# Kernel tuning notes

Measured on AMD Instinct MI355X. Metric: run time of the kernel, lower is better.

The kernel has to match this reference:

```python
import jax, jax.numpy as jnp
import numpy as np

N = 50000      # nodes
E = 800000     # edges (avg degree 16)
D_IN = 128
D_H = 128
D_OUT = 64
SLOPE = 0.2    # leaky-relu negative slope (from the 0.2 constants in the graph)


def setup_inputs() -> dict:
    key = jax.random.key(0)
    ks = jax.random.split(key, 18)
    def w(k, shape, fan_in):
        return jax.random.normal(k, shape, jnp.float32) / np.sqrt(fan_in)
    inp = {
        "x": jax.random.normal(ks[0], (N, D_IN), jnp.float32),
        "W0": w(ks[1], (D_IN, D_H), D_IN),
        "b0": jnp.zeros((D_H,), jnp.float32),
        "Wq1": w(ks[2], (D_H, D_H), D_H),
        "bq1": jnp.zeros((D_H,), jnp.float32),
        "Wp1": w(ks[3], (D_H, D_H), D_H),
        "bp1": jnp.zeros((D_H,), jnp.float32),
        "a1": 0.1 * w(ks[4], (D_H,), D_H),
        "bg2": jnp.zeros((D_H,), jnp.float32),
        "Wq2": w(ks[5], (D_H, D_OUT), D_H),
        "bq2": jnp.zeros((D_OUT,), jnp.float32),
        "Wp2": w(ks[6], (D_H, D_OUT), D_H),
        "bp2": jnp.zeros((D_OUT,), jnp.float32),
        "a2": 0.1 * w(ks[7], (D_OUT,), D_OUT),
        "b_out": jnp.zeros((D_OUT,), jnp.float32),
        "src": jax.random.randint(ks[8], (E,), 0, N),
        "dst": jax.random.randint(ks[9], (E,), 0, N),
        "num_nodes": N,
    }
    return inp


def _gat_block(m, src, dst, Wq, bq, Wp, bp, a, n):
    # m: [N, d_in]; q/p: [N, d]
    q = m @ Wq + bq
    p = m @ Wp + bp
    # edge scores: s_e = sum_d leaky_relu(q[dst_e] + p[src_e]) * a_d   [E]
    e = jax.nn.leaky_relu(q[dst] + p[src], SLOPE)          # [E, d]
    s = jnp.einsum("ed,d->e", e, a)                        # [E]
    es = jnp.exp(s)                                        # unstabilized exp, as in source graph
    denom = jax.ops.segment_sum(es, dst, num_segments=n)   # [N]
    alpha = es / denom[dst]                                # [E] edge softmax over incoming edges
    # aggregate messages alpha_e * p[src_e] into dst nodes
    agg = jax.ops.segment_sum(alpha[:, None] * p[src], dst, num_segments=n)  # [N, d]
    return agg


def reference(x, W0, b0, Wq1, bq1, Wp1, bp1, a1, bg2, Wq2, bq2, Wp2, bp2, a2, b_out, src, dst, num_nodes):
    m1 = jax.nn.gelu(x @ W0 + b0, approximate=False)       # erf GELU per graph constants
    h1 = _gat_block(m1, src, dst, Wq1, bq1, Wp1, bp1, a1, num_nodes)
    m2 = jax.nn.gelu(h1 + bg2, approximate=False)
    h2 = _gat_block(m2, src, dst, Wq2, bq2, Wp2, bp2, a2, num_nodes)
    return h2 + b_out
```

## Files before the change

kernel.cpp:

```cpp
#include <hip/hip_runtime.h>
#include <hip/hip_bf16.h>
#include <math.h>


#define SLOPE 0.2f

typedef __attribute__((ext_vector_type(8))) __bf16 bf16x8;
typedef __attribute__((ext_vector_type(4))) float f32x4;

__device__ __forceinline__ float gelu_erf(float x) {
    return 0.5f * x * (1.0f + erff(x * 0.70710678118654752f));
}

__device__ __forceinline__ unsigned short f2bf(float f) {
    unsigned int u = __float_as_uint(f);
    return (unsigned short)((u + 0x7fffu + ((u >> 16) & 1u)) >> 16);
}
__device__ __forceinline__ float bf2f(unsigned short h) {
    return __uint_as_float((unsigned int)h << 16);
}

__device__ __forceinline__ float row16_sum(float x) {
    x += __int_as_float(__builtin_amdgcn_update_dpp(0, __float_as_int(x), 0x121, 0xF, 0xF, true));
    x += __int_as_float(__builtin_amdgcn_update_dpp(0, __float_as_int(x), 0x122, 0xF, 0xF, true));
    x += __int_as_float(__builtin_amdgcn_update_dpp(0, __float_as_int(x), 0x124, 0xF, 0xF, true));
    x += __int_as_float(__builtin_amdgcn_update_dpp(0, __float_as_int(x), 0x128, 0xF, 0xF, true));
    return x;
}

__device__ __forceinline__ int swz(int off) { return off ^ ((off >> 4) & 0x70); }

__global__ __launch_bounds__(256) void pack_w(
    const float* __restrict__ W0,  const float* __restrict__ Wq1,
    const float* __restrict__ Wp1, const float* __restrict__ Wq2,
    const float* __restrict__ Wp2,
    unsigned short* __restrict__ P0,  unsigned short* __restrict__ Pq1,
    unsigned short* __restrict__ Pp1, unsigned short* __restrict__ Pq2,
    unsigned short* __restrict__ Pp2)
{
    const float* W; unsigned short* P; int C;
    switch (blockIdx.y) {
        case 0:  W = W0;  P = P0;  C = 128; break;
        case 1:  W = Wq1; P = Pq1; C = 128; break;
        case 2:  W = Wp1; P = Pp1; C = 128; break;
        case 3:  W = Wq2; P = Pq2; C = 64;  break;
        default: W = Wp2; P = Pp2; C = 64;  break;
    }
    int i = blockIdx.x * 256 + threadIdx.x;
    int CE = C * 128;
    if (i >= CE) return;
    int j = i & 7, l = (i >> 3) & 63, ks = (i >> 9) & 3, ct = i >> 11;
    int k = ks * 32 + ((l >> 4) << 3) + j;
    int n = ct * 16 + (l & 15);
    float v = W[k * C + n];
    unsigned short hb = f2bf(v);
    P[i] = hb;
    P[CE + i] = f2bf(v - bf2f(hb));
}

template <int C, bool TWO, int EPI>
__global__ __launch_bounds__(256) void mfma_gemm(
    const float* __restrict__ Af,
    const unsigned short* __restrict__ AHg, const unsigned short* __restrict__ ALg,
    const unsigned short* __restrict__ P1, const float* __restrict__ b1,
    const unsigned short* __restrict__ P2, const float* __restrict__ b2,
    float* __restrict__ outq, unsigned short* __restrict__ outp,
    unsigned short* __restrict__ o1hi, unsigned short* __restrict__ o1lo,
    int N)
{
    constexpr int CE  = C * 128;
    constexpr int CTT = (TWO ? 2 : 1) * (C / 16);
    constexpr int CTW = CTT / 4;
    constexpr int QCT = C / 16;

    __shared__ __align__(16) unsigned char lds[32768];

    const int t = threadIdx.x;
    const int lane = t & 63;
    const int w = t >> 6;
    const int row0 = blockIdx.x * 64;
    const int mcol = lane & 15;
    const int hk = lane >> 4;

    if constexpr (EPI == 0) {
#pragma unroll
        for (int i = 0; i < 8; i++) {
            int idx = t + i * 256;
            int row = idx >> 5;
            int gr = row0 + row;
            float4 v = make_float4(0.f, 0.f, 0.f, 0.f);
            if (gr < N) v = *reinterpret_cast<const float4*>(Af + (size_t)gr * 128 + (idx & 31) * 4);
            const float* f = reinterpret_cast<const float*>(&v);
            unsigned int h[4], l[4];
#pragma unroll
            for (int j = 0; j < 4; j++) {
                unsigned short hb = f2bf(f[j]);
                h[j] = hb;
                l[j] = f2bf(f[j] - bf2f(hb));
            }
            int so = swz(row * 256 + (idx & 31) * 8);
            *reinterpret_cast<uint2*>(&lds[so])         = make_uint2(h[0] | (h[1] << 16), h[2] | (h[3] << 16));
            *reinterpret_cast<uint2*>(&lds[16384 + so]) = make_uint2(l[0] | (l[1] << 16), l[2] | (l[3] << 16));
        }
    } else {
#pragma unroll
        for (int i = 0; i < 4; i++) {
            int idx = t + i * 256;
            int row = idx >> 4;
            int gr = row0 + row;
            uint4 vh = make_uint4(0, 0, 0, 0), vl = make_uint4(0, 0, 0, 0);
            if (gr < N) {
                vh = *reinterpret_cast<const uint4*>(AHg + (size_t)gr * 128 + (idx & 15) * 8);
                vl = *reinterpret_cast<const uint4*>(ALg + (size_t)gr * 128 + (idx & 15) * 8);
            }
            int so = swz(row * 256 + (idx & 15) * 16);
            *reinterpret_cast<uint4*>(&lds[so])         = vh;
            *reinterpret_cast<uint4*>(&lds[16384 + so]) = vl;
        }
    }
    __syncthreads();

    f32x4 acc[CTW][4];
#pragma unroll
    for (int c = 0; c < CTW; c++)
#pragma unroll
        for (int rf = 0; rf < 4; rf++) acc[c][rf] = (f32x4){0.f, 0.f, 0.f, 0.f};

#pragma unroll
    for (int ks = 0; ks < 4; ks++) {
        bf16x8 ah[4], al[4];
#pragma unroll
        for (int rf = 0; rf < 4; rf++) {
            int so = swz((rf * 16 + mcol) * 256 + ks * 64 + hk * 16);
            ah[rf] = *reinterpret_cast<const bf16x8*>(&lds[so]);
            al[rf] = *reinterpret_cast<const bf16x8*>(&lds[16384 + so]);
        }
#pragma unroll
        for (int c = 0; c < CTW; c++) {
            int ctg = w * CTW + c;
            bool isq = (!TWO) || (ctg < QCT);
            int ct = isq ? ctg : ctg - QCT;
            const unsigned short* P = isq ? P1 : P2;
            const unsigned short* Wp = P + ((ct * 4 + ks) * 64 + lane) * 8;
            bf16x8 bh = *reinterpret_cast<const bf16x8*>(Wp);
            bf16x8 bl = *reinterpret_cast<const bf16x8*>(Wp + CE);
#pragma unroll
            for (int rf = 0; rf < 4; rf++) {
                acc[c][rf] = __builtin_amdgcn_mfma_f32_16x16x32_bf16(ah[rf], bh, acc[c][rf], 0, 0, 0);
                acc[c][rf] = __builtin_amdgcn_mfma_f32_16x16x32_bf16(al[rf], bh, acc[c][rf], 0, 0, 0);
                acc[c][rf] = __builtin_amdgcn_mfma_f32_16x16x32_bf16(ah[rf], bl, acc[c][rf], 0, 0, 0);
            }
        }
    }

    __syncthreads();

    if constexpr (EPI == 0) {
#pragma unroll
        for (int c = 0; c < CTW; c++) {
            int col = (w * CTW + c) * 16 + mcol;
            float bv = b1[col];
#pragma unroll
            for (int rf = 0; rf < 4; rf++) {
#pragma unroll
                for (int r = 0; r < 4; r++) {
                    int row = rf * 16 + hk * 4 + r;
                    float v = gelu_erf(acc[c][rf][r] + bv);
                    unsigned short hb = f2bf(v);
                    int bo = row * 256 + col * 2;
                    *reinterpret_cast<unsigned short*>(&lds[swz(bo)])         = hb;
                    *reinterpret_cast<unsigned short*>(&lds[16384 + swz(bo)]) = f2bf(v - bf2f(hb));
                }
            }
        }
        __syncthreads();
#pragma unroll
        for (int i = 0; i < 8; i++) {
            int idx = t + i * 256;
            int pl = idx >> 10;
            int j = idx & 1023;
            int row = j >> 4;
            int gr = row0 + row;
            if (gr < N) {
                uint4 v = *reinterpret_cast<const uint4*>(&lds[pl * 16384 + swz(row * 256 + (j & 15) * 16)]);
                unsigned short* dp = pl ? o1lo : o1hi;
                *reinterpret_cast<uint4*>(dp + (size_t)gr * 128 + (j & 15) * 8) = v;
            }
        }
    } else {
#pragma unroll
        for (int c = 0; c < CTW; c++) {
            int ctg = w * CTW + c;
            bool isq = ctg < QCT;
            int ct = isq ? ctg : ctg - QCT;
            int col = ct * 16 + mcol;
            float bv = (isq ? b1 : b2)[col];
#pragma unroll
            for (int rf = 0; rf < 4; rf++) {
#pragma unroll
                for (int r = 0; r < 4; r++) {
                    int row = rf * 16 + hk * 4 + r;
                    int gr = row0 + row;
                    float v = acc[c][rf][r] + bv;
                    if (isq) {
                        if (gr < N) outq[(size_t)gr * C + col] = v;
                    } else {
                        *reinterpret_cast<unsigned short*>(&lds[swz(row * 256 + col * 2)]) = f2bf(v);
                    }
                }
            }
        }
        __syncthreads();
        constexpr int SLOTS = C / 8;
#pragma unroll
        for (int i = 0; i < (64 * SLOTS) / 256; i++) {
            int idx = t + i * 256;
            int row = idx / SLOTS;
            int sl = idx % SLOTS;
            int gr = row0 + row;
            if (gr < N)
                *reinterpret_cast<uint4*>(outp + (size_t)gr * C + sl * 8) =
                    *reinterpret_cast<const uint4*>(&lds[swz(row * 256 + sl * 16)]);
        }
    }
}


__global__ __launch_bounds__(256) void hist_coarse(
    const int* __restrict__ dst, int* __restrict__ gh, int E, int CB)
{
    __shared__ int cnt[4096];
    const int blk = blockIdx.x;
    const int t = threadIdx.x;
    for (int b = t; b < CB; b += 256) cnt[b] = 0;
    __syncthreads();
    const int epb = (E + 63) / 64;
    const int s = blk * epb;
    const int e_ = (s + epb < E) ? s + epb : E;
    for (int i = s + t; i < e_; i += 256)
        atomicAdd(&cnt[dst[i] >> 4], 1);
    __syncthreads();
    for (int b = t; b < CB; b += 256)
        gh[b * 64 + blk] = cnt[b];
}

__global__ __launch_bounds__(256) void scan1_kernel(const int* __restrict__ gh,
                                                    int* __restrict__ gscan,
                                                    int* __restrict__ bsum, int M)
{
    __shared__ int lds[256];
    int t = threadIdx.x;
    int i = blockIdx.x * 256 + t;
    int v = (i < M) ? gh[i] : 0;
    lds[t] = v;
    __syncthreads();
    int x = v;
    for (int off = 1; off < 256; off <<= 1) {
        int y = (t >= off) ? lds[t - off] : 0;
        __syncthreads();
        x += y;
        lds[t] = x;
        __syncthreads();
    }
    if (i < M) gscan[i] = x - v;
    if (t == 255) bsum[blockIdx.x] = x;
}

__global__ __launch_bounds__(1024) void scan2_kernel(int* __restrict__ bsum, int NB)
{
    __shared__ int lds[1024];
    int t = threadIdx.x;
    int v = (t < NB) ? bsum[t] : 0;
    lds[t] = v;
    __syncthreads();
    int x = v;
    for (int off = 1; off < 1024; off <<= 1) {
        int y = (t >= off) ? lds[t - off] : 0;
        __syncthreads();
        x += y;
        lds[t] = x;
        __syncthreads();
    }
    if (t < NB) bsum[t] = x - v;
}

__global__ __launch_bounds__(256) void scan3_kernel(int* __restrict__ gscan,
                                                    const int* __restrict__ bsum, int M)
{
    int i = blockIdx.x * 256 + threadIdx.x;
    if (i < M) gscan[i] += bsum[blockIdx.x];
}

__global__ __launch_bounds__(256) void scatter_coarse(
    const int* __restrict__ src, const int* __restrict__ dst,
    const int* __restrict__ gscan, int2* __restrict__ pairs, int E, int CB)
{
    __shared__ int cur[4096];
    const int blk = blockIdx.x;
    const int t = threadIdx.x;
    for (int b = t; b < CB; b += 256)
        cur[b] = gscan[b * 64 + blk];
    __syncthreads();
    const int epb = (E + 63) / 64;
    const int s = blk * epb;
    const int e_ = (s + epb < E) ? s + epb : E;
    for (int i = s + t; i < e_; i += 256) {
        int d = dst[i];
        int sv = src[i];
        int pos = atomicAdd(&cur[d >> 4], 1);
        pairs[pos] = make_int2(d, sv);
    }
}

__global__ __launch_bounds__(256) void finalize_kernel(
    const int2* __restrict__ pairs, const int* __restrict__ gscan,
    int* __restrict__ offs, int* __restrict__ csr_src, int N, int E, int CB)
{
    const int c = blockIdx.x;
    const int t = threadIdx.x;
    __shared__ unsigned int cnt[8], rnk[8];
    __shared__ int pref[16];
    if (t < 8) { cnt[t] = 0u; rnk[t] = 0u; }
    __syncthreads();

    const int s  = gscan[c * 64];
    const int e_ = (c + 1 < CB) ? gscan[(c + 1) * 64] : E;
    const int base = c * 16;

    for (int i = s + t; i < e_; i += 256) {
        int d = pairs[i].x - base;
        atomicAdd(&cnt[d >> 1], 1u << ((d & 1) * 16));
    }
    __syncthreads();
    if (t == 0) {
        int run = s;
        for (int j = 0; j < 16; j++) {
            pref[j] = run;
            run += (int)((cnt[j >> 1] >> ((j & 1) * 16)) & 0xffffu);
        }
    }
    __syncthreads();
    if (t < 16 && base + t < N) offs[base + t] = pref[t];
    if (c == CB - 1 && t == 0) offs[N] = E;

    for (int i = s + t; i < e_; i += 256) {
        int2 pr = pairs[i];
        int d = pr.x - base;
        unsigned int old = atomicAdd(&rnk[d >> 1], 1u << ((d & 1) * 16));
        int r = (int)((old >> ((d & 1) * 16)) & 0xffffu);
        csr_src[pref[d] + r] = pr.y;
    }
}

template <int D, int EPI>
__global__ __launch_bounds__(256) void gat_agg(
    const float* __restrict__ q, const unsigned short* __restrict__ p,
    const float* __restrict__ a, const float* __restrict__ bvec,
    const int* __restrict__ offs, const int* __restrict__ csr_src,
    float* __restrict__ out, unsigned short* __restrict__ mhi,
    unsigned short* __restrict__ mlo, int N)
{
    constexpr int VPL = D / 16;
    const int t = threadIdx.x;
    const int lane = t & 63;
    const int sl = lane & 15;
    const int base = sl * VPL;
    const int node = blockIdx.x * 16 + ((t >> 6) << 2) + (lane >> 4);
    const bool valid = node < N;

    float qv[VPL], a6[VPL], a4[VPL], acc[VPL];
#pragma unroll
    for (int v = 0; v < VPL; v++) { qv[v] = 0.f; acc[v] = 0.f; }
    if (valid) {
        const float* qp = q + (size_t)node * D + base;
        float4 q0 = *reinterpret_cast<const float4*>(qp);
        qv[0] = q0.x; qv[1] = q0.y; qv[2] = q0.z; qv[3] = q0.w;
        if constexpr (VPL == 8) {
            float4 q1 = *reinterpret_cast<const float4*>(qp + 4);
            qv[4] = q1.x; qv[5] = q1.y; qv[6] = q1.z; qv[7] = q1.w;
        }
    }
#pragma unroll
    for (int v = 0; v < VPL; v++) {
        float av = a[base + v];
        a6[v] = 0.6f * av;
        a4[v] = 0.4f * av;
    }

    float denom = 0.f;
    int e  = valid ? offs[node] : 0;
    int e1 = valid ? offs[node + 1] : 0;

    int s0 = csr_src[(e + 0 < e1) ? e + 0 : 0];
    int s1 = csr_src[(e + 1 < e1) ? e + 1 : 0];
    int s2 = csr_src[(e + 2 < e1) ? e + 2 : 0];
    int s3 = csr_src[(e + 3 < e1) ? e + 3 : 0];

    float pv[4][VPL];

    while (__any(e < e1)) {
        const bool a0 = (e + 0) < e1, a1b = (e + 1) < e1,
                   a2 = (e + 2) < e1, a3 = (e + 3) < e1;

        if constexpr (D == 128) {
            uint4 u0 = *reinterpret_cast<const uint4*>(p + (size_t)s0 * 128 + base);
            uint4 u1 = *reinterpret_cast<const uint4*>(p + (size_t)s1 * 128 + base);
            uint4 u2 = *reinterpret_cast<const uint4*>(p + (size_t)s2 * 128 + base);
            uint4 u3 = *reinterpret_cast<const uint4*>(p + (size_t)s3 * 128 + base);
            pv[0][0] = __uint_as_float(u0.x << 16); pv[0][1] = __uint_as_float(u0.x & 0xffff0000u);
            pv[0][2] = __uint_as_float(u0.y << 16); pv[0][3] = __uint_as_float(u0.y & 0xffff0000u);
            pv[0][4] = __uint_as_float(u0.z << 16); pv[0][5] = __uint_as_float(u0.z & 0xffff0000u);
            pv[0][6] = __uint_as_float(u0.w << 16); pv[0][7] = __uint_as_float(u0.w & 0xffff0000u);
            pv[1][0] = __uint_as_float(u1.x << 16); pv[1][1] = __uint_as_float(u1.x & 0xffff0000u);
            pv[1][2] = __uint_as_float(u1.y << 16); pv[1][3] = __uint_as_float(u1.y & 0xffff0000u);
            pv[1][4] = __uint_as_float(u1.z << 16); pv[1][5] = __uint_as_float(u1.z & 0xffff0000u);
            pv[1][6] = __uint_as_float(u1.w << 16); pv[1][7] = __uint_as_float(u1.w & 0xffff0000u);
            pv[2][0] = __uint_as_float(u2.x << 16); pv[2][1] = __uint_as_float(u2.x & 0xffff0000u);
            pv[2][2] = __uint_as_float(u2.y << 16); pv[2][3] = __uint_as_float(u2.y & 0xffff0000u);
            pv[2][4] = __uint_as_float(u2.z << 16); pv[2][5] = __uint_as_float(u2.z & 0xffff0000u);
            pv[2][6] = __uint_as_float(u2.w << 16); pv[2][7] = __uint_as_float(u2.w & 0xffff0000u);
            pv[3][0] = __uint_as_float(u3.x << 16); pv[3][1] = __uint_as_float(u3.x & 0xffff0000u);
            pv[3][2] = __uint_as_float(u3.y << 16); pv[3][3] = __uint_as_float(u3.y & 0xffff0000u);
            pv[3][4] = __uint_as_float(u3.z << 16); pv[3][5] = __uint_as_float(u3.z & 0xffff0000u);
            pv[3][6] = __uint_as_float(u3.w << 16); pv[3][7] = __uint_as_float(u3.w & 0xffff0000u);
        } else {
            uint2 u0 = *reinterpret_cast<const uint2*>(p + (size_t)s0 * 64 + base);
            uint2 u1 = *reinterpret_cast<const uint2*>(p + (size_t)s1 * 64 + base);
            uint2 u2 = *reinterpret_cast<const uint2*>(p + (size_t)s2 * 64 + base);
            uint2 u3 = *reinterpret_cast<const uint2*>(p + (size_t)s3 * 64 + base);
            pv[0][0] = __uint_as_float(u0.x << 16); pv[0][1] = __uint_as_float(u0.x & 0xffff0000u);
            pv[0][2] = __uint_as_float(u0.y << 16); pv[0][3] = __uint_as_float(u0.y & 0xffff0000u);
            pv[1][0] = __uint_as_float(u1.x << 16); pv[1][1] = __uint_as_float(u1.x & 0xffff0000u);
            pv[1][2] = __uint_as_float(u1.y << 16); pv[1][3] = __uint_as_float(u1.y & 0xffff0000u);
            pv[2][0] = __uint_as_float(u2.x << 16); pv[2][1] = __uint_as_float(u2.x & 0xffff0000u);
            pv[2][2] = __uint_as_float(u2.y << 16); pv[2][3] = __uint_as_float(u2.y & 0xffff0000u);
            pv[3][0] = __uint_as_float(u3.x << 16); pv[3][1] = __uint_as_float(u3.x & 0xffff0000u);
            pv[3][2] = __uint_as_float(u3.y << 16); pv[3][3] = __uint_as_float(u3.y & 0xffff0000u);
        }

        const int en = e + 4;
        const int n0 = csr_src[(en + 0 < e1) ? en + 0 : 0];
        const int n1 = csr_src[(en + 1 < e1) ? en + 1 : 0];
        const int n2 = csr_src[(en + 2 < e1) ? en + 2 : 0];
        const int n3 = csr_src[(en + 3 < e1) ? en + 3 : 0];

        float pa0 = 0.f, pa1 = 0.f, pa2 = 0.f, pa3 = 0.f;
#pragma unroll
        for (int v = 0; v < VPL; v++) {
            float d0 = qv[v] + pv[0][v];
            float d1 = qv[v] + pv[1][v];
            float d2 = qv[v] + pv[2][v];
            float d3 = qv[v] + pv[3][v];
            pa0 = fmaf(d0, a6[v], pa0); pa0 = fmaf(fabsf(d0), a4[v], pa0);
            pa1 = fmaf(d1, a6[v], pa1); pa1 = fmaf(fabsf(d1), a4[v], pa1);
            pa2 = fmaf(d2, a6[v], pa2); pa2 = fmaf(fabsf(d2), a4[v], pa2);
            pa3 = fmaf(d3, a6[v], pa3); pa3 = fmaf(fabsf(d3), a4[v], pa3);
        }

        float r0 = row16_sum(pa0);
        float r1 = row16_sum(pa1);
        float r2 = row16_sum(pa2);
        float r3 = row16_sum(pa3);

        float esm0 = a0  ? __expf(r0) : 0.f;
        float esm1 = a1b ? __expf(r1) : 0.f;
        float esm2 = a2  ? __expf(r2) : 0.f;
        float esm3 = a3  ? __expf(r3) : 0.f;
        denom += (esm0 + esm1) + (esm2 + esm3);
#pragma unroll
        for (int v = 0; v < VPL; v++) {
            acc[v] = fmaf(esm0, pv[0][v], acc[v]);
            acc[v] = fmaf(esm1, pv[1][v], acc[v]);
            acc[v] = fmaf(esm2, pv[2][v], acc[v]);
            acc[v] = fmaf(esm3, pv[3][v], acc[v]);
        }

        e = en;
        s0 = n0; s1 = n1; s2 = n2; s3 = n3;
    }

    if (!valid) return;
    float inv = (denom != 0.f) ? 1.f / denom : 0.f;
    if constexpr (EPI == 0) {
        union { unsigned short us[8]; uint4 v; } H, L;
#pragma unroll
        for (int v = 0; v < VPL; v++) {
            float g = gelu_erf(acc[v] * inv + bvec[base + v]);
            H.us[v] = f2bf(g);
            L.us[v] = f2bf(g - bf2f(H.us[v]));
        }
        *reinterpret_cast<uint4*>(mhi + (size_t)node * 128 + base) = H.v;
        *reinterpret_cast<uint4*>(mlo + (size_t)node * 128 + base) = L.v;
    } else {
        union { float f[4]; float4 v; } O;
#pragma unroll
        for (int v = 0; v < VPL; v++) O.f[v] = acc[v] * inv + bvec[base + v];
        *reinterpret_cast<float4*>(out + (size_t)node * D + base) = O.v;
    }
}

extern "C" void kernel_launch(void* const* d_in, const int* in_sizes, int n_in,
                              void* d_out, int out_size, void* d_ws, size_t ws_size,
                              hipStream_t stream)
{
    const float* x     = (const float*)d_in[0];
    const float* W0    = (const float*)d_in[1];
    const float* b0    = (const float*)d_in[2];
    const float* Wq1   = (const float*)d_in[3];
    const float* bq1   = (const float*)d_in[4];
    const float* Wp1   = (const float*)d_in[5];
    const float* bp1   = (const float*)d_in[6];
    const float* a1    = (const float*)d_in[7];
    const float* bg2   = (const float*)d_in[8];
    const float* Wq2   = (const float*)d_in[9];
    const float* bq2   = (const float*)d_in[10];
    const float* Wp2   = (const float*)d_in[11];
    const float* bp2   = (const float*)d_in[12];
    const float* a2    = (const float*)d_in[13];
    const float* b_out = (const float*)d_in[14];
    const int*   src   = (const int*)d_in[15];
    const int*   dst   = (const int*)d_in[16];

    const int N = in_sizes[0] / 128;
    const int E = in_sizes[15];
    float* out = (float*)d_out;

    float* q_buf        = (float*)d_ws;
    unsigned short* pb  = (unsigned short*)(q_buf + (size_t)N * 128);
    unsigned short* Mhi = pb + (size_t)N * 128;
    unsigned short* Mlo = Mhi + (size_t)N * 128;
    unsigned short* P0  = Mlo + (size_t)N * 128;
    unsigned short* Pq1 = P0  + 128 * 128 * 2;
    unsigned short* Pp1 = Pq1 + 128 * 128 * 2;
    unsigned short* Pq2 = Pp1 + 128 * 128 * 2;
    unsigned short* Pp2 = Pq2 + 128 * 64 * 2;
    int* offs    = (int*)(Pp2 + 128 * 64 * 2);
    int* csr_src = offs + (N + 2);
    const int CB = (N + 15) / 16;
    const int M  = CB * 64;
    int* gh    = csr_src + E;
    int* gscan = gh + M;
    int* bsum  = gscan + M;
    int2* pairs = (int2*)q_buf;

    const int NB1 = (M + 255) / 256;

    pack_w<<<dim3(64, 5), 256, 0, stream>>>(W0, Wq1, Wp1, Wq2, Wp2,
                                            P0, Pq1, Pp1, Pq2, Pp2);
    hist_coarse<<<64, 256, 0, stream>>>(dst, gh, E, CB);
    scan1_kernel<<<NB1, 256, 0, stream>>>(gh, gscan, bsum, M);
    scan2_kernel<<<1, 1024, 0, stream>>>(bsum, NB1);
    scan3_kernel<<<NB1, 256, 0, stream>>>(gscan, bsum, M);
    scatter_coarse<<<64, 256, 0, stream>>>(src, dst, gscan, pairs, E, CB);
    finalize_kernel<<<CB, 256, 0, stream>>>(pairs, gscan, offs, csr_src, N, E, CB);

    const int GB64 = (N + 63) / 64;
    const int GGAT = (N + 15) / 16;

    mfma_gemm<128, false, 0><<<GB64, 256, 0, stream>>>(
        x, nullptr, nullptr, P0, b0, nullptr, nullptr,
        nullptr, nullptr, Mhi, Mlo, N);
    mfma_gemm<128, true, 1><<<GB64, 256, 0, stream>>>(
        nullptr, Mhi, Mlo, Pq1, bq1, Pp1, bp1,
        q_buf, pb, nullptr, nullptr, N);
    gat_agg<128, 0><<<GGAT, 256, 0, stream>>>(
        q_buf, pb, a1, bg2, offs, csr_src,
        nullptr, Mhi, Mlo, N);
    mfma_gemm<64, true, 1><<<GB64, 256, 0, stream>>>(
        nullptr, Mhi, Mlo, Pq2, bq2, Pp2, bp2,
        q_buf, pb, nullptr, nullptr, N);
    gat_agg<64, 1><<<GGAT, 256, 0, stream>>>(
        q_buf, pb, a2, b_out, offs, csr_src,
        out, nullptr, nullptr, N);
}
```

Baseline: 284.6 us.

## Sort nodes by in-degree into a permutation to balance GAT aggregation work

Builds a degree-bucketed node permutation: finalize counts nodes per (clamped degree, block-index low bits) bucket, a single-block scan turns the counts into offsets, and a scatter kernel writes the permuted node list. Both gat_agg launches then index nodes through this permutation. Each wavefront therefore handles nodes of similar degree, which reduces divergence and idle lanes caused by uneven edge counts. The cost is two extra small launches plus atomics, and the reordering loses the locality of consecutive node IDs for q reads and output writes.

```diff
diff --git a/kernel.cpp b/kernel.cpp
--- a/kernel.cpp
+++ b/kernel.cpp
@@ -227,11 +227,14 @@
 
 
 __global__ __launch_bounds__(256) void hist_coarse(
-    const int* __restrict__ dst, int* __restrict__ gh, int E, int CB)
+    const int* __restrict__ dst, int* __restrict__ gh, int* __restrict__ dbkt,
+    int E, int CB)
 {
     __shared__ int cnt[4096];
     const int blk = blockIdx.x;
     const int t = threadIdx.x;
+    if (blk == 0)
+        for (int b = t; b < 512; b += 256) dbkt[b] = 0;
     for (int b = t; b < CB; b += 256) cnt[b] = 0;
     __syncthreads();
     const int epb = (E + 63) / 64;
@@ -314,7 +317,8 @@
 
 __global__ __launch_bounds__(256) void finalize_kernel(
     const int2* __restrict__ pairs, const int* __restrict__ gscan,
-    int* __restrict__ offs, int* __restrict__ csr_src, int N, int E, int CB)
+    int* __restrict__ offs, int* __restrict__ csr_src, int* __restrict__ dbkt,
+    int N, int E, int CB)
 {
     const int c = blockIdx.x;
     const int t = threadIdx.x;
@@ -340,7 +344,12 @@
         }
     }
     __syncthreads();
-    if (t < 16 && base + t < N) offs[base + t] = pref[t];
+    if (t < 16 && base + t < N) {
+        offs[base + t] = pref[t];
+        int deg = (int)((cnt[t >> 1] >> ((t & 1) * 16)) & 0xffffu);
+        int b = ((deg < 63 ? deg : 63) << 3) | (c & 7);
+        atomicAdd(&dbkt[b], 1);
+    }
     if (c == CB - 1 && t == 0) offs[N] = E;
 
     for (int i = s + t; i < e_; i += 256) {
@@ -352,11 +361,42 @@
     }
 }
 
+__global__ __launch_bounds__(512) void scan_dbkt(int* __restrict__ dbkt)
+{
+    __shared__ int lds[512];
+    int t = threadIdx.x;
+    int v = dbkt[t];
+    lds[t] = v;
+    __syncthreads();
+    int x = v;
+    for (int off = 1; off < 512; off <<= 1) {
+        int y = (t >= off) ? lds[t - off] : 0;
+        __syncthreads();
+        x += y;
+        lds[t] = x;
+        __syncthreads();
+    }
+    dbkt[t] = x - v;
+}
+
+__global__ __launch_bounds__(256) void scatter_perm(
+    const int* __restrict__ offs, int* __restrict__ dbkt,
+    int* __restrict__ perm, int N)
+{
+    int n = blockIdx.x * 256 + threadIdx.x;
+    if (n >= N) return;
+    int deg = offs[n + 1] - offs[n];
+    int b = ((deg < 63 ? deg : 63) << 3) | ((n >> 4) & 7);
+    int pos = atomicAdd(&dbkt[b], 1);
+    perm[pos] = n;
+}
+
 template <int D, int EPI>
 __global__ __launch_bounds__(256) void gat_agg(
     const float* __restrict__ q, const unsigned short* __restrict__ p,
     const float* __restrict__ a, const float* __restrict__ bvec,
     const int* __restrict__ offs, const int* __restrict__ csr_src,
+    const int* __restrict__ perm,
     float* __restrict__ out, unsigned short* __restrict__ mhi,
     unsigned short* __restrict__ mlo, int N)
 {
@@ -365,8 +405,9 @@
     const int lane = t & 63;
     const int sl = lane & 15;
     const int base = sl * VPL;
-    const int node = blockIdx.x * 16 + ((t >> 6) << 2) + (lane >> 4);
-    const bool valid = node < N;
+    const int nidx = blockIdx.x * 16 + ((t >> 6) << 2) + (lane >> 4);
+    const bool valid = nidx < N;
+    const int node = valid ? perm[nidx] : 0;
 
     float qv[VPL], a6[VPL], a4[VPL], acc[VPL];
 #pragma unroll
@@ -541,18 +582,22 @@
     int* gh    = csr_src + E;
     int* gscan = gh + M;
     int* bsum  = gscan + M;
+    int* dbkt  = bsum + 1024;
+    int* perm  = dbkt + 512;
     int2* pairs = (int2*)q_buf;
 
     const int NB1 = (M + 255) / 256;
 
     pack_w<<<dim3(64, 5), 256, 0, stream>>>(W0, Wq1, Wp1, Wq2, Wp2,
                                             P0, Pq1, Pp1, Pq2, Pp2);
-    hist_coarse<<<64, 256, 0, stream>>>(dst, gh, E, CB);
+    hist_coarse<<<64, 256, 0, stream>>>(dst, gh, dbkt, E, CB);
     scan1_kernel<<<NB1, 256, 0, stream>>>(gh, gscan, bsum, M);
     scan2_kernel<<<1, 1024, 0, stream>>>(bsum, NB1);
     scan3_kernel<<<NB1, 256, 0, stream>>>(gscan, bsum, M);
     scatter_coarse<<<64, 256, 0, stream>>>(src, dst, gscan, pairs, E, CB);
-    finalize_kernel<<<CB, 256, 0, stream>>>(pairs, gscan, offs, csr_src, N, E, CB);
+    finalize_kernel<<<CB, 256, 0, stream>>>(pairs, gscan, offs, csr_src, dbkt, N, E, CB);
+    scan_dbkt<<<1, 512, 0, stream>>>(dbkt);
+    scatter_perm<<<(N + 255) / 256, 256, 0, stream>>>(offs, dbkt, perm, N);
 
     const int GB64 = (N + 63) / 64;
     const int GGAT = (N + 15) / 16;
@@ -564,12 +609,12 @@
         nullptr, Mhi, Mlo, Pq1, bq1, Pp1, bp1,
         q_buf, pb, nullptr, nullptr, N);
     gat_agg<128, 0><<<GGAT, 256, 0, stream>>>(
-        q_buf, pb, a1, bg2, offs, csr_src,
+        q_buf, pb, a1, bg2, offs, csr_src, perm,
         nullptr, Mhi, Mlo, N);
     mfma_gemm<64, true, 1><<<GB64, 256, 0, stream>>>(
         nullptr, Mhi, Mlo, Pq2, bq2, Pp2, bp2,
         q_buf, pb, nullptr, nullptr, N);
     gat_agg<64, 1><<<GGAT, 256, 0, stream>>>(
-        q_buf, pb, a2, b_out, offs, csr_src,
+        q_buf, pb, a2, b_out, offs, csr_src, perm,
         out, nullptr, nullptr, N);
 }
```

Result: slower. 466.5 us (+64.0%).

## Rewrite CSR finalize as one wavefront per bucket using ballot ranking

Applied to the files above, without the earlier changes.

The finalize kernel now handles each 16-node bucket with a single 64-lane wavefront, four buckets per block, in place of one 256-thread block per bucket. Per-node counts and ranks inside each bucket come from wave ballots and popcounts, replacing LDS atomics and __syncthreads. This is meant to cut block-level sync and atomic contention in a small preprocessing kernel. Within-bucket order becomes deterministic. Each chunk of 64 edges costs 16 ballots.

```diff
diff --git a/kernel.cpp b/kernel.cpp
--- a/kernel.cpp
+++ b/kernel.cpp
@@ -316,39 +316,56 @@
     const int2* __restrict__ pairs, const int* __restrict__ gscan,
     int* __restrict__ offs, int* __restrict__ csr_src, int N, int E, int CB)
 {
-    const int c = blockIdx.x;
-    const int t = threadIdx.x;
-    __shared__ unsigned int cnt[8], rnk[8];
-    __shared__ int pref[16];
-    if (t < 8) { cnt[t] = 0u; rnk[t] = 0u; }
-    __syncthreads();
-
-    const int s  = gscan[c * 64];
-    const int e_ = (c + 1 < CB) ? gscan[(c + 1) * 64] : E;
-    const int base = c * 16;
-
-    for (int i = s + t; i < e_; i += 256) {
-        int d = pairs[i].x - base;
-        atomicAdd(&cnt[d >> 1], 1u << ((d & 1) * 16));
-    }
-    __syncthreads();
-    if (t == 0) {
-        int run = s;
+    const int wid = blockIdx.x * 4 + (threadIdx.x >> 6);
+    const int lane = threadIdx.x & 63;
+    if (wid >= CB) return;
+
+    const int s    = gscan[wid * 64];
+    const int e_   = (wid + 1 < CB) ? gscan[(wid + 1) * 64] : E;
+    const int base = wid * 16;
+    const unsigned long long ltmask = (lane == 63) ? ~0ull >> 1
+                                                   : (1ull << lane) - 1ull;
+
+    int rc[16];
+#pragma unroll
+    for (int j = 0; j < 16; j++) rc[j] = 0;
+    for (int c0 = s; c0 < e_; c0 += 64) {
+        int i = c0 + lane;
+        int d = (i < e_) ? pairs[i].x - base : -1;
+#pragma unroll
+        for (int j = 0; j < 16; j++)
+            rc[j] += (int)__popcll(__ballot(d == j));
+    }
+
+    int pref[16];
+    int run = s;
+#pragma unroll
+    for (int j = 0; j < 16; j++) { pref[j] = run; run += rc[j]; }
+    int pref_v = 0;
+#pragma unroll
+    for (int j = 0; j < 16; j++) pref_v = (lane == j) ? pref[j] : pref_v;
+
+    if (lane < 16 && base + lane < N) offs[base + lane] = pref_v;
+    if (wid == CB - 1 && lane == 16) offs[N] = E;
+
+    int rcv = 0;
+    for (int c0 = s; c0 < e_; c0 += 64) {
+        int i = c0 + lane;
+        const bool act = i < e_;
+        int2 pr = act ? pairs[i] : make_int2(base - 1, 0);
+        int d = pr.x - base;
+        unsigned long long msel = 0;
+        int addcnt = 0;
+#pragma unroll
         for (int j = 0; j < 16; j++) {
-            pref[j] = run;
-            run += (int)((cnt[j >> 1] >> ((j & 1) * 16)) & 0xffffu);
-        }
-    }
-    __syncthreads();
-    if (t < 16 && base + t < N) offs[base + t] = pref[t];
-    if (c == CB - 1 && t == 0) offs[N] = E;
-
-    for (int i = s + t; i < e_; i += 256) {
-        int2 pr = pairs[i];
-        int d = pr.x - base;
-        unsigned int old = atomicAdd(&rnk[d >> 1], 1u << ((d & 1) * 16));
-        int r = (int)((old >> ((d & 1) * 16)) & 0xffffu);
-        csr_src[pref[d] + r] = pr.y;
+            unsigned long long m = __ballot(d == j);
+            if (d == j) msel = m;
+            if (lane == j) addcnt = (int)__popcll(m);
+        }
+        int subrank = (int)__popcll(msel & ltmask);
+        int posbase = __builtin_amdgcn_ds_bpermute(d * 4, pref_v + rcv);
+        if (act) csr_src[posbase + subrank] = pr.y;
+        rcv += addcnt;
     }
 }
 
@@ -552,7 +569,7 @@
     scan2_kernel<<<1, 1024, 0, stream>>>(bsum, NB1);
     scan3_kernel<<<NB1, 256, 0, stream>>>(gscan, bsum, M);
     scatter_coarse<<<64, 256, 0, stream>>>(src, dst, gscan, pairs, E, CB);
-    finalize_kernel<<<CB, 256, 0, stream>>>(pairs, gscan, offs, csr_src, N, E, CB);
+    finalize_kernel<<<(CB + 3) / 4, 256, 0, stream>>>(pairs, gscan, offs, csr_src, N, E, CB);
 
     const int GB64 = (N + 63) / 64;
     const int GGAT = (N + 15) / 16;
```

New measurement: 290.6 us. 1.02x slower.
